# Kernel optimization log

Hardware: AMD Instinct MI355X
Metric: run time of the kernel (lower is better)

Reference implementation:

```python
import jax, jax.numpy as jnp
import numpy as np
import math

B, T, C = 4, 2048, 1024
H, D = 16, 64            # num_heads, head_dim
ORIG_LEN = 4096
MIN_FREQ, MAX_FREQ = 0.5, 40.0


def setup_inputs() -> dict:
    key = jax.random.key(0)
    ks = jax.random.split(key, 6)
    x = jax.random.normal(ks[0], (B, T, C), dtype=jnp.float32)
    keep_idx = jnp.sort(jax.random.randint(ks[1], (B, T, 1), 0, ORIG_LEN), axis=1)
    W_qkv = jax.random.normal(ks[2], (C, 3 * C), dtype=jnp.float32) * (1.0 / math.sqrt(C))
    b_qkv = jnp.zeros((3 * C,), dtype=jnp.float32)
    W_proj = jax.random.normal(ks[3], (C, C), dtype=jnp.float32) * (1.0 / math.sqrt(C))
    b_proj = jnp.zeros((C,), dtype=jnp.float32)
    return {"x": x, "keep_idx": keep_idx, "original_seq_len": ORIG_LEN,
            "W_qkv": W_qkv, "b_qkv": b_qkv, "W_proj": W_proj, "b_proj": b_proj}


def _rope_angles(positions, orig_len):
    # positions: [b, t] float token positions in the ORIGINAL sequence.
    # golden_gate 1-D RoPE: normalized positions times geometric frequency band.
    half = D // 2
    freqs = MIN_FREQ * (MAX_FREQ / MIN_FREQ) ** (jnp.arange(half, dtype=jnp.float32) / (half - 1))
    pos_norm = positions / jnp.float32(orig_len)          # [b, t]
    return 2.0 * jnp.pi * pos_norm[:, :, None] * freqs    # [b, t, half]


def _apply_rope(x, cos, sin):
    # x: [b, h, t, d]; cos/sin: [b, 1, t, d/2]; rotate (first half, second half) pairs
    half = D // 2
    x1, x2 = x[..., :half], x[..., half:]
    return jnp.concatenate([x1 * cos - x2 * sin, x1 * sin + x2 * cos], axis=-1)


def reference(x, keep_idx, original_seq_len, W_qkv, b_qkv, W_proj, b_proj):
    b, t, c = x.shape
    # fused QKV projection + head split: (b,t,3c) -> (b,t,3,h,d) -> (b,h,t,3,d)
    qkv = (x @ W_qkv + b_qkv).reshape(b, t, 3, H, D).transpose(0, 3, 1, 2, 4)
    q, k, v = qkv[:, :, :, 0], qkv[:, :, :, 1], qkv[:, :, :, 2]  # each [b,h,t,d]

    positions = keep_idx[..., 0].astype(jnp.float32)             # [b, t]
    ang = _rope_angles(positions, original_seq_len)              # [b, t, d/2]
    cos = jnp.cos(ang)[:, None]                                  # [b,1,t,d/2]
    sin = jnp.sin(ang)[:, None]
    q = _apply_rope(q, cos, sin)
    k = _apply_rope(k, cos, sin)

    # dense non-causal scaled dot-product attention
    scale = 1.0 / math.sqrt(D)
    scores = jnp.einsum('bhqd,bhkd->bhqk', q, k) * scale
    attn = jax.nn.softmax(scores, axis=-1)
    out = jnp.einsum('bhqk,bhkd->bhqd', attn, v)                 # [b,h,t,d]

    out = out.transpose(0, 2, 1, 3).reshape(b, t, H * D)         # [b,t,c]
    return out @ W_proj + b_proj
```

## Files before the change

kernel.cpp:

```cpp
#include <hip/hip_runtime.h>
#include <hip/hip_bf16.h>
#include <math.h>

#define B_ 4
#define T_ 2048
#define C_ 1024
#define H_ 16
#define D_ 64

typedef __attribute__((ext_vector_type(8))) short bf16x8_t;
typedef __attribute__((ext_vector_type(4))) float f32x4_t;
typedef __attribute__((ext_vector_type(2))) unsigned int uiv2_t;

#define SHIFT2 32.0f

#define GLOAD_LDS16(gp, lp)                                                          \
    __builtin_amdgcn_global_load_lds(                                                \
        (const __attribute__((address_space(1))) void*)(gp),                         \
        (__attribute__((address_space(3))) void*)(lp), 16, 0, 0)

#define WAVE_ORDER() __builtin_amdgcn_wave_barrier()

__device__ inline unsigned int pack2bf(float a, float b) {
    __hip_bfloat162 h = __float22bfloat162_rn(make_float2(a, b));
    return *reinterpret_cast<unsigned int*>(&h);
}

__global__ __launch_bounds__(256)
void prep_kernel(const float* __restrict__ x, __hip_bfloat16* __restrict__ xbf,
                 const int* __restrict__ keep, const int* __restrict__ orig,
                 float* __restrict__ tab,
                 const float* __restrict__ Wqkv, __hip_bfloat16* __restrict__ WqkvT,
                 const float* __restrict__ Wproj, __hip_bfloat16* __restrict__ WprojT) {
    __shared__ float s[32][33];
    const int bid = blockIdx.x;
    const int tid = threadIdx.x;

    if (bid < 8192) {
        int i = bid * 256 + tid;
        float4 v = *(const float4*)(x + (size_t)i * 4);
        uint2 u;
        u.x = pack2bf(v.x, v.y);
        u.y = pack2bf(v.z, v.w);
        *(uint2*)(xbf + (size_t)i * 4) = u;
    } else if (bid < 9216) {
        int i = (bid - 8192) * 256 + tid;
        int tok = i >> 5, d = i & 31;
        float freq = 0.5f * exp2f((float)d * (6.321928094887362f / 31.0f));
        float ang  = 6.283185307179586f * ((float)keep[tok] / (float)(*orig)) * freq;
        tab[(size_t)tok * 64 + d]      = cosf(ang);
        tab[(size_t)tok * 64 + 32 + d] = sinf(ang);
    } else {
        const float* in;
        __hip_bfloat16* outp;
        int N, n0, k0, r;
        if (bid < 12288) {
            r = bid - 9216;
            in = Wqkv; outp = WqkvT; N = 3 * C_;
            n0 = (r % 96) * 32; k0 = (r / 96) * 32;
        } else {
            r = bid - 12288;
            in = Wproj; outp = WprojT; N = C_;
            n0 = (r % 32) * 32; k0 = (r / 32) * 32;
        }
        const int K = C_;
        const int tx = tid & 31;
        const int ty = tid >> 5;
#pragma unroll
        for (int yy = 0; yy < 32; yy += 8)
            s[ty + yy][tx] = in[(size_t)(k0 + ty + yy) * N + n0 + tx];
        __syncthreads();
#pragma unroll
        for (int yy = 0; yy < 32; yy += 8)
            outp[(size_t)(n0 + ty + yy) * K + k0 + tx] = __float2bfloat16(s[tx][ty + yy]);
    }
}

#define ATILE (256 * 32)
#define BTILE (128 * 32)

template <int MODE>
__global__ __launch_bounds__(512)
void gemm_kernel(const __hip_bfloat16* __restrict__ A,
                 const __hip_bfloat16* __restrict__ BT,
                 const float* __restrict__ bias,
                 float* __restrict__ out,
                 __hip_bfloat16* __restrict__ qbuf,
                 __hip_bfloat16* __restrict__ kbuf,
                 __hip_bfloat16* __restrict__ vtbuf,
                 const float* __restrict__ ropetab,
                 int M, int N, int K) {
    __shared__ __align__(16) __hip_bfloat16 GS[3 * ATILE + 3 * BTILE];

    const int tid  = threadIdx.x;
    const int lane = tid & 63;
    const int wave = tid >> 6;
    const int wm   = wave >> 1;
    const int wn   = wave & 1;
    const int l15  = lane & 15;
    const int quad = lane >> 4;

    const int nT  = N >> 7;
    const int grp = blockIdx.x / (8 * nT);
    const int rem = blockIdx.x - grp * 8 * nT;
    const int m0  = (grp * 8 + (rem & 7)) * 256;
    const int n0  = (rem >> 3) * 128;

    f32x4_t acc[4][4];
#pragma unroll
    for (int i = 0; i < 4; i++)
#pragma unroll
        for (int j = 0; j < 4; j++) acc[i][j] = (f32x4_t)0.0f;

    const int lrow = lane >> 2;
    const int scol = ((lane & 3) ^ ((lane >> 4) & 3)) * 8;
    const __hip_bfloat16* gA  = A  + (size_t)(m0 + wave * 32 + lrow) * K + scol;
    const __hip_bfloat16* gA2 = gA + (size_t)16 * K;
    const __hip_bfloat16* gB  = BT + (size_t)(n0 + wave * 16 + lrow) * K + scol;
    const int ldsA = wave * 32 * 32;
    const int ldsB = wave * 16 * 32;

    const int NK = K >> 5;
    GLOAD_LDS16(gA,  GS + ldsA);
    GLOAD_LDS16(gA2, GS + ldsA + 16 * 32);
    GLOAD_LDS16(gB,  GS + 3 * ATILE + ldsB);
    if (NK > 1) {
        GLOAD_LDS16(gA  + 32, GS + ATILE + ldsA);
        GLOAD_LDS16(gA2 + 32, GS + ATILE + ldsA + 16 * 32);
        GLOAD_LDS16(gB  + 32, GS + 3 * ATILE + BTILE + ldsB);
    }

    int cur = 0;
    int pre = 2;
    for (int t = 0; t < NK; ++t) {
        if (t + 1 < NK) {
            asm volatile("s_waitcnt vmcnt(3)" ::: "memory");
        } else {
            asm volatile("s_waitcnt vmcnt(0)" ::: "memory");
        }
        __builtin_amdgcn_s_barrier();
        __builtin_amdgcn_sched_barrier(0);

        if (t + 2 < NK) {
            const int kk = (t + 2) << 5;
            GLOAD_LDS16(gA  + kk, GS + pre * ATILE + ldsA);
            GLOAD_LDS16(gA2 + kk, GS + pre * ATILE + ldsA + 16 * 32);
            GLOAD_LDS16(gB  + kk, GS + 3 * ATILE + pre * BTILE + ldsB);
            __builtin_amdgcn_sched_barrier(0);
        }

        const int Ab = cur * ATILE;
        const int Bb = 3 * ATILE + cur * BTILE;
        bf16x8_t af[4], bfv[4];
#pragma unroll
        for (int i = 0; i < 4; i++)
            af[i] = *(const bf16x8_t*)(GS + Ab + (wm * 64 + i * 16 + l15) * 32 +
                                       ((quad ^ (l15 >> 2)) * 8));
#pragma unroll
        for (int j = 0; j < 4; j++)
            bfv[j] = *(const bf16x8_t*)(GS + Bb + (wn * 64 + j * 16 + l15) * 32 +
                                        ((quad ^ (l15 >> 2)) * 8));
#pragma unroll
        for (int i = 0; i < 4; i++)
#pragma unroll
            for (int j = 0; j < 4; j++)
                acc[i][j] = __builtin_amdgcn_mfma_f32_16x16x32_bf16(af[i], bfv[j], acc[i][j], 0, 0, 0);

        cur = (cur == 2) ? 0 : cur + 1;
        pre = (pre == 2) ? 0 : pre + 1;
    }

    float bv[4];
#pragma unroll
    for (int j = 0; j < 4; j++)
        bv[j] = bias[n0 + wn * 64 + j * 16 + l15];

    if (MODE == 0) {
#pragma unroll
        for (int i = 0; i < 4; i++)
#pragma unroll
            for (int r = 0; r < 4; r++) {
                int row = m0 + wm * 64 + i * 16 + quad * 4 + r;
#pragma unroll
                for (int j = 0; j < 4; j++) {
                    int col = n0 + wn * 64 + j * 16 + l15;
                    out[(size_t)row * N + col] = acc[i][j][r] + bv[j];
                }
            }
    } else {
        const int cb   = n0 + wn * 64;
        const int part = cb >> 10;
        if (part == 2) {
            __syncthreads();
            const int hb = (n0 & 1023) >> 6;
            const int bb = m0 >> 11;
            const int t0 = m0 & 2047;
            __hip_bfloat16* L = GS;
#pragma unroll
            for (int p = 0; p < 2; ++p) {
                if ((wm >> 1) == p) {
#pragma unroll
                    for (int j = 0; j < 4; j++) {
                        int d = wn * 64 + j * 16 + l15;
#pragma unroll
                        for (int i = 0; i < 4; i++) {
                            int rtb = (wm & 1) * 64 + i * 16 + quad * 4;
                            uint2 pk;
                            pk.x = pack2bf(acc[i][j][0] + bv[j], acc[i][j][1] + bv[j]);
                            pk.y = pack2bf(acc[i][j][2] + bv[j], acc[i][j][3] + bv[j]);
                            *(uint2*)(L + d * 136 + rtb) = pk;
                        }
                    }
                }
                __syncthreads();
                {
                    int row = tid >> 2;
                    int hb2 = hb + (row >> 6);
                    int dd  = row & 63;
                    const __hip_bfloat16* src = L + row * 136;
                    __hip_bfloat16* dstv = vtbuf +
                        ((size_t)((bb * H_ + hb2) * D_ + dd)) * T_ + t0 + p * 128;
#pragma unroll
                    for (int s2 = 0; s2 < 4; s2++) {
                        int ch = (tid & 3) + s2 * 4;
                        *(bf16x8_t*)(dstv + ch * 8) = *(const bf16x8_t*)(src + ch * 8);
                    }
                }
                if (p == 0) __syncthreads();
            }
        } else {
            const int h = (cb & 1023) >> 6;
            __hip_bfloat16* dst = (part == 0) ? qbuf : kbuf;
            const float sc = (part == 0) ? 0.18033688011112042f : 1.0f;
#pragma unroll
            for (int i = 0; i < 4; i++) {
#pragma unroll
                for (int r = 0; r < 4; r++) {
                    int row = m0 + wm * 64 + i * 16 + quad * 4 + r;
                    int b = row >> 11;
                    int t = row & 2047;
                    const float* trow = ropetab + (size_t)row * 64;
                    size_t base = ((size_t)(b * H_ + h) * T_ + t) * D_;
#pragma unroll
                    for (int j = 0; j < 2; j++) {
                        int d = j * 16 + l15;
                        float cs = trow[d];
                        float sn = trow[32 + d];
                        float x1 = acc[i][j][r]     + bv[j];
                        float x2 = acc[i][j + 2][r] + bv[j + 2];
                        dst[base + d]      = __float2bfloat16(sc * (x1 * cs - x2 * sn));
                        dst[base + d + 32] = __float2bfloat16(sc * (x1 * sn + x2 * cs));
                    }
                }
            }
        }
    }
}

#define KVTILE (64 * 64)

__global__ __launch_bounds__(256, 4)
void attn_kernel(const __hip_bfloat16* __restrict__ q,
                 const __hip_bfloat16* __restrict__ k,
                 const __hip_bfloat16* __restrict__ vt,
                 __hip_bfloat16* __restrict__ attn_out) {
    __shared__ __align__(16) __hip_bfloat16 SMEM[4 * KVTILE];

    const int tid  = threadIdx.x;
    const int lane = tid & 63;
    const int wave = tid >> 6;
    const int l15  = lane & 15;
    const int quad = lane >> 4;
    const int x7   = l15 & 7;

    const int bh = blockIdx.x & 63;
    const int qt = blockIdx.x >> 6;
    const int b  = bh >> 4;
    const int h  = bh & 15;

    const size_t qkbase = (size_t)bh * T_ * D_;
    const size_t vbase  = (size_t)bh * D_ * T_;
    const int    qrow0  = qt * 128 + wave * 32;

    const int drow   = lane >> 3;
    const int gchunk = (lane & 7) ^ drow;

    const __hip_bfloat16* kg = k + qkbase;
    const __hip_bfloat16* vg = vt + vbase;

    const int c0 = ((quad)     ^ x7) * 8;
    const int c1 = ((4 + quad) ^ x7) * 8;

    bf16x8_t qa[2][2];
#pragma unroll
    for (int qf = 0; qf < 2; qf++)
#pragma unroll
        for (int kk = 0; kk < 2; kk++)
            qa[qf][kk] = *(const bf16x8_t*)(q + qkbase +
                          (size_t)(qrow0 + qf * 16 + l15) * D_ + kk * 32 + quad * 8);

    bf16x8_t ones;
#pragma unroll
    for (int i = 0; i < 8; i++) ones[i] = (short)0x3F80;

    const f32x4_t mbias = (f32x4_t)(-SHIFT2);

    f32x4_t o[2][4];
#pragma unroll
    for (int qf = 0; qf < 2; qf++)
#pragma unroll
        for (int jd = 0; jd < 4; jd++) o[qf][jd] = (f32x4_t)0.0f;
    f32x4_t osum[2];
    osum[0] = (f32x4_t)0.0f;
    osum[1] = (f32x4_t)0.0f;

#pragma unroll
    for (int i = 0; i < 2; i++) {
        int r = wave * 16 + i * 8;
        GLOAD_LDS16(kg + (size_t)(r + drow) * D_ + gchunk * 8, SMEM + r * 64);
        GLOAD_LDS16(vg + (size_t)(r + drow) * T_ + gchunk * 8, SMEM + 2 * KVTILE + r * 64);
    }

    for (int kt = 0; kt < T_ / 64; kt++) {
        const int curoff = (kt & 1) * KVTILE;
        const int nxtoff = curoff ^ KVTILE;

        asm volatile("s_waitcnt vmcnt(0)" ::: "memory");
        __builtin_amdgcn_s_barrier();
        __builtin_amdgcn_sched_barrier(0);

        if (kt + 1 < T_ / 64) {
#pragma unroll
            for (int i = 0; i < 2; i++) {
                int r = wave * 16 + i * 8;
                GLOAD_LDS16(kg + (size_t)((kt + 1) * 64 + r + drow) * D_ + gchunk * 8,
                            SMEM + nxtoff + r * 64);
                GLOAD_LDS16(vg + (size_t)(r + drow) * T_ + (kt + 1) * 64 + gchunk * 8,
                            SMEM + 2 * KVTILE + nxtoff + r * 64);
            }
            __builtin_amdgcn_sched_barrier(0);
        }

        const __hip_bfloat16* KLc = SMEM + curoff;
        const __hip_bfloat16* VLc = SMEM + 2 * KVTILE + curoff;

        bf16x8_t kf[4][2];
#pragma unroll
        for (int jt = 0; jt < 4; jt++) {
            kf[jt][0] = *(const bf16x8_t*)(KLc + (jt * 16 + l15) * 64 + c0);
            kf[jt][1] = *(const bf16x8_t*)(KLc + (jt * 16 + l15) * 64 + c1);
        }

        f32x4_t sT[2][4];
        __builtin_amdgcn_s_setprio(1);
#pragma unroll
        for (int jt = 0; jt < 4; jt++)
#pragma unroll
            for (int qf = 0; qf < 2; qf++) {
                sT[qf][jt] = __builtin_amdgcn_mfma_f32_16x16x32_bf16(
                    kf[jt][0], qa[qf][0], mbias, 0, 0, 0);
                sT[qf][jt] = __builtin_amdgcn_mfma_f32_16x16x32_bf16(
                    kf[jt][1], qa[qf][1], sT[qf][jt], 0, 0, 0);
            }
        __builtin_amdgcn_s_setprio(0);

        bf16x8_t pb[2][2];
#pragma unroll
        for (int qf = 0; qf < 2; qf++) {
            unsigned int w0[4], w1[4];
#pragma unroll
            for (int jt = 0; jt < 4; jt++) {
                float p0 = __builtin_amdgcn_exp2f(sT[qf][jt][0]);
                float p1 = __builtin_amdgcn_exp2f(sT[qf][jt][1]);
                float p2 = __builtin_amdgcn_exp2f(sT[qf][jt][2]);
                float p3 = __builtin_amdgcn_exp2f(sT[qf][jt][3]);
                w0[jt] = pack2bf(p0, p1);
                w1[jt] = pack2bf(p2, p3);
            }
#pragma unroll
            for (int kk = 0; kk < 2; kk++) {
                uiv2_t s0 = __builtin_amdgcn_permlane32_swap(w0[2 * kk], w0[2 * kk + 1], false, false);
                uiv2_t r0 = __builtin_amdgcn_permlane16_swap(s0[0], s0[1], false, false);
                uiv2_t s1 = __builtin_amdgcn_permlane32_swap(w1[2 * kk], w1[2 * kk + 1], false, false);
                uiv2_t r1 = __builtin_amdgcn_permlane16_swap(s1[0], s1[1], false, false);
                union { unsigned int u[4]; bf16x8_t v; } pu;
                pu.u[0] = r0[0];
                pu.u[1] = r1[0];
                pu.u[2] = r0[1];
                pu.u[3] = r1[1];
                pb[qf][kk] = pu.v;
            }
        }

        __builtin_amdgcn_s_setprio(1);
#pragma unroll
        for (int qf = 0; qf < 2; qf++) {
            osum[qf] = __builtin_amdgcn_mfma_f32_16x16x32_bf16(ones, pb[qf][0], osum[qf], 0, 0, 0);
            osum[qf] = __builtin_amdgcn_mfma_f32_16x16x32_bf16(ones, pb[qf][1], osum[qf], 0, 0, 0);
        }

#pragma unroll
        for (int jd = 0; jd < 4; jd++) {
            bf16x8_t vf0 = *(const bf16x8_t*)(VLc + (jd * 16 + l15) * 64 + c0);
            bf16x8_t vf1 = *(const bf16x8_t*)(VLc + (jd * 16 + l15) * 64 + c1);
#pragma unroll
            for (int qf = 0; qf < 2; qf++) {
                o[qf][jd] = __builtin_amdgcn_mfma_f32_16x16x32_bf16(vf0, pb[qf][0], o[qf][jd], 0, 0, 0);
                o[qf][jd] = __builtin_amdgcn_mfma_f32_16x16x32_bf16(vf1, pb[qf][1], o[qf][jd], 0, 0, 0);
            }
        }
        __builtin_amdgcn_s_setprio(0);
    }

    float inv[2];
    inv[0] = 1.0f / osum[0][0];
    inv[1] = 1.0f / osum[1][0];

    __syncthreads();
    __hip_bfloat16* Pep = SMEM + wave * (32 * 72);

#pragma unroll
    for (int qf = 0; qf < 2; qf++) {
#pragma unroll
        for (int jd = 0; jd < 4; jd++) {
            uint2 pk;
            pk.x = pack2bf(o[qf][jd][0] * inv[qf], o[qf][jd][1] * inv[qf]);
            pk.y = pack2bf(o[qf][jd][2] * inv[qf], o[qf][jd][3] * inv[qf]);
            *(uint2*)(Pep + (qf * 16 + l15) * 72 + jd * 16 + quad * 4) = pk;
        }
    }
    WAVE_ORDER();

#pragma unroll
    for (int rnd = 0; rnd < 4; rnd++) {
        int row = rnd * 8 + (lane >> 3);
        int col = (lane & 7) * 8;
        bf16x8_t vrow = *(const bf16x8_t*)(Pep + row * 72 + col);
        int token = qt * 128 + wave * 32 + row;
        *(bf16x8_t*)(attn_out + ((size_t)(b * T_ + token)) * C_ + h * 64 + col) = vrow;
    }
}

extern "C" void kernel_launch(void* const* d_in, const int* in_sizes, int n_in,
                              void* d_out, int out_size, void* d_ws, size_t ws_size,
                              hipStream_t stream) {
    const float* x        = (const float*)d_in[0];
    const int*   keep_idx = (const int*)d_in[1];
    const int*   orig_len = (const int*)d_in[2];
    const float* Wqkv     = (const float*)d_in[3];
    const float* bqkv     = (const float*)d_in[4];
    const float* Wproj    = (const float*)d_in[5];
    const float* bproj    = (const float*)d_in[6];
    float*       out      = (float*)d_out;

    const size_t NTOK = (size_t)B_ * T_;
    const size_t QKV1 = NTOK * C_;

    __hip_bfloat16* qbuf    = (__hip_bfloat16*)d_ws;
    __hip_bfloat16* kbuf    = qbuf    + QKV1;
    __hip_bfloat16* vtbuf   = kbuf    + QKV1;
    __hip_bfloat16* attnbuf = vtbuf   + QKV1;
    __hip_bfloat16* WqkvT   = attnbuf + QKV1;
    __hip_bfloat16* WprojT  = WqkvT   + (size_t)C_ * 3 * C_;
    __hip_bfloat16* xbf     = WprojT  + (size_t)C_ * C_;
    float*          ropetab = (float*)(xbf + QKV1);

    prep_kernel<<<13312, 256, 0, stream>>>(x, xbf, keep_idx, orig_len, ropetab,
                                           Wqkv, WqkvT, Wproj, WprojT);

    gemm_kernel<1><<<(8192 / 256) * (3072 / 128), 512, 0, stream>>>(
        xbf, WqkvT, bqkv, nullptr, qbuf, kbuf, vtbuf, ropetab, 8192, 3072, 1024);

    attn_kernel<<<(T_ / 128) * 64, 256, 0, stream>>>(qbuf, kbuf, vtbuf, attnbuf);

    gemm_kernel<0><<<(8192 / 256) * (1024 / 128), 512, 0, stream>>>(
        attnbuf, WprojT, bproj, out, nullptr, nullptr, nullptr, nullptr, 8192, 1024, 1024);
}
```

Baseline: 262.1 us.

## Widen attention blocks to 8 waves and deepen K/V prefetch to four stages

The attention kernel now runs 512 threads per block covering 256 query rows, so each K/V tile loaded into LDS is shared by twice as many waves. The K/V pipeline grows from double buffering to a 4-slot ring with loads issued three tiles ahead, and partial vmcnt waits replace the full drain. The aim is to halve global K/V traffic per query and hide load latency better. In exchange LDS per block grows to 64KB, which may cut resident blocks per CU, and the grid shrinks to 512 blocks.

Result: no change. 258.3 us (median of 3 runs) (-1.4%).

```diff
diff --git a/kernel.cpp b/kernel.cpp
--- a/kernel.cpp
+++ b/kernel.cpp
@@ -257,14 +257,14 @@
     }
 }
 
-#define KVTILE (64 * 64)
-
-__global__ __launch_bounds__(256, 4)
+#define KVT 4096
+
+__global__ __launch_bounds__(512, 4)
 void attn_kernel(const __hip_bfloat16* __restrict__ q,
                  const __hip_bfloat16* __restrict__ k,
                  const __hip_bfloat16* __restrict__ vt,
                  __hip_bfloat16* __restrict__ attn_out) {
-    __shared__ __align__(16) __hip_bfloat16 SMEM[4 * KVTILE];
+    __shared__ __align__(16) __hip_bfloat16 SMEM[8 * KVT];
 
     const int tid  = threadIdx.x;
     const int lane = tid & 63;
@@ -280,10 +280,11 @@
 
     const size_t qkbase = (size_t)bh * T_ * D_;
     const size_t vbase  = (size_t)bh * D_ * T_;
-    const int    qrow0  = qt * 128 + wave * 32;
+    const int    qrow0  = qt * 256 + wave * 32;
 
     const int drow   = lane >> 3;
     const int gchunk = (lane & 7) ^ drow;
+    const int r      = wave * 8;
 
     const __hip_bfloat16* kg = k + qkbase;
     const __hip_bfloat16* vg = vt + vbase;
@@ -315,34 +316,36 @@
     osum[1] = (f32x4_t)0.0f;
 
 #pragma unroll
-    for (int i = 0; i < 2; i++) {
-        int r = wave * 16 + i * 8;
-        GLOAD_LDS16(kg + (size_t)(r + drow) * D_ + gchunk * 8, SMEM + r * 64);
-        GLOAD_LDS16(vg + (size_t)(r + drow) * T_ + gchunk * 8, SMEM + 2 * KVTILE + r * 64);
-    }
-
-    for (int kt = 0; kt < T_ / 64; kt++) {
-        const int curoff = (kt & 1) * KVTILE;
-        const int nxtoff = curoff ^ KVTILE;
-
-        asm volatile("s_waitcnt vmcnt(0)" ::: "memory");
+    for (int tt = 0; tt < 3; ++tt) {
+        GLOAD_LDS16(kg + (size_t)(tt * 64 + r + drow) * D_ + gchunk * 8,
+                    SMEM + tt * KVT + r * 64);
+        GLOAD_LDS16(vg + (size_t)(r + drow) * T_ + tt * 64 + gchunk * 8,
+                    SMEM + 4 * KVT + tt * KVT + r * 64);
+    }
+
+    const int NT = T_ / 64;
+    for (int kt = 0; kt < NT; kt++) {
+        if (kt + 2 < NT) {
+            asm volatile("s_waitcnt vmcnt(4)" ::: "memory");
+        } else if (kt + 1 < NT) {
+            asm volatile("s_waitcnt vmcnt(2)" ::: "memory");
+        } else {
+            asm volatile("s_waitcnt vmcnt(0)" ::: "memory");
+        }
         __builtin_amdgcn_s_barrier();
         __builtin_amdgcn_sched_barrier(0);
 
-        if (kt + 1 < T_ / 64) {
-#pragma unroll
-            for (int i = 0; i < 2; i++) {
-                int r = wave * 16 + i * 8;
-                GLOAD_LDS16(kg + (size_t)((kt + 1) * 64 + r + drow) * D_ + gchunk * 8,
-                            SMEM + nxtoff + r * 64);
-                GLOAD_LDS16(vg + (size_t)(r + drow) * T_ + (kt + 1) * 64 + gchunk * 8,
-                            SMEM + 2 * KVTILE + nxtoff + r * 64);
-            }
+        if (kt + 3 < NT) {
+            const int slot = (kt + 3) & 3;
+            GLOAD_LDS16(kg + (size_t)((kt + 3) * 64 + r + drow) * D_ + gchunk * 8,
+                        SMEM + slot * KVT + r * 64);
+            GLOAD_LDS16(vg + (size_t)(r + drow) * T_ + (kt + 3) * 64 + gchunk * 8,
+                        SMEM + 4 * KVT + slot * KVT + r * 64);
             __builtin_amdgcn_sched_barrier(0);
         }
 
-        const __hip_bfloat16* KLc = SMEM + curoff;
-        const __hip_bfloat16* VLc = SMEM + 2 * KVTILE + curoff;
+        const __hip_bfloat16* KLc = SMEM + (kt & 3) * KVT;
+        const __hip_bfloat16* VLc = SMEM + 4 * KVT + (kt & 3) * KVT;
 
         bf16x8_t kf[4][2];
 #pragma unroll
@@ -436,7 +439,7 @@
         int row = rnd * 8 + (lane >> 3);
         int col = (lane & 7) * 8;
         bf16x8_t vrow = *(const bf16x8_t*)(Pep + row * 72 + col);
-        int token = qt * 128 + wave * 32 + row;
+        int token = qt * 256 + wave * 32 + row;
         *(bf16x8_t*)(attn_out + ((size_t)(b * T_ + token)) * C_ + h * 64 + col) = vrow;
     }
 }
@@ -471,7 +474,7 @@
     gemm_kernel<1><<<(8192 / 256) * (3072 / 128), 512, 0, stream>>>(
         xbf, WqkvT, bqkv, nullptr, qbuf, kbuf, vtbuf, ropetab, 8192, 3072, 1024);
 
-    attn_kernel<<<(T_ / 128) * 64, 256, 0, stream>>>(qbuf, kbuf, vtbuf, attnbuf);
+    attn_kernel<<<(T_ / 256) * 64, 512, 0, stream>>>(qbuf, kbuf, vtbuf, attnbuf);
 
     gemm_kernel<0><<<(8192 / 256) * (1024 / 128), 512, 0, stream>>>(
         attnbuf, WprojT, bproj, out, nullptr, nullptr, nullptr, nullptr, 8192, 1024, 1024);
```
